# Kernel optimization log

Hardware: AMD Instinct MI355X
Metric: run time of the kernel (lower is better)

## Reference

```python
import jax, jax.numpy as jnp
import numpy as np

N = 100000   # num nodes (in_channels)
D = 128      # out_channels
H = 2 * D    # hidden dim
E = 1600000  # num edges


def gcn_conv(x, W, b, src, dst, dinv):
    """PyG GCNConv: linear -> symmetric-normalized aggregation (with self loops) -> +bias."""
    xw = x @ W                                   # [N, out]
    norm = dinv[src] * dinv[dst]                 # [E]
    msg = xw[src] * norm[:, None]                # [E, out]  gather + scale
    agg = jax.ops.segment_sum(msg, dst, num_segments=N)  # scatter-add to targets
    agg = agg + xw * (dinv * dinv)[:, None]      # self-loop contribution
    return agg + b


def setup_inputs() -> dict:
    key = jax.random.key(0)
    k1, k2, k3, k4, k5, k6 = jax.random.split(key, 6)
    emb = jax.random.normal(k1, (N, D), dtype=jnp.float32)
    # Glorot-ish scaled weights
    W1 = jax.random.normal(k2, (D, H), dtype=jnp.float32) * (1.0 / np.sqrt(D))
    b1 = jnp.zeros((H,), dtype=jnp.float32)
    W2 = jax.random.normal(k3, (H, D), dtype=jnp.float32) * (1.0 / np.sqrt(H))
    b2 = jnp.zeros((D,), dtype=jnp.float32)
    edge_index = jax.random.randint(k4, (2, E), 0, N, dtype=jnp.int32).astype(jnp.int64)
    return {"emb": emb, "W1": W1, "b1": b1, "W2": W2, "b2": b2, "edge_index": edge_index}


def reference(emb, W1, b1, W2, b2, edge_index):
    src = edge_index[0]
    dst = edge_index[1]
    # degrees include the self loop added by GCNConv (add_self_loops=True)
    deg = jax.ops.segment_sum(jnp.ones((E,), dtype=emb.dtype), dst, num_segments=N) + 1.0
    dinv = jax.lax.rsqrt(deg)                    # deg >= 1, always finite
    x = gcn_conv(emb, W1, b1, src, dst, dinv)    # [N, 2D]
    x = jax.nn.relu(x)
    out = gcn_conv(x, W2, b2, src, dst, dinv)    # [N, D]
    return out
```

## Files before the change

### kernel.cpp

```cpp
#include <hip/hip_runtime.h>
#include <hip/hip_bf16.h>

#define NN 100000
#define DD 128
#define HH 256

#define NBKT 391
#define ABLK 256

typedef _Float16 half_t;
typedef _Float16 half8 __attribute__((ext_vector_type(8)));
typedef _Float16 half4_t __attribute__((ext_vector_type(4)));
typedef float floatx4 __attribute__((ext_vector_type(4)));


__global__ __launch_bounds__(256) void hist_bkt(const int* __restrict__ dst,
                                                int* __restrict__ cnt,
                                                int* __restrict__ tot,
                                                int E, int epb) {
    __shared__ int h[NBKT];
    for (int i = threadIdx.x; i < NBKT; i += 256) h[i] = 0;
    __syncthreads();
    int base = blockIdx.x * epb;
    int end = min(base + epb, E);
    for (int e = base + (int)threadIdx.x; e < end; e += 256)
        atomicAdd(&h[dst[e] >> 8], 1);
    __syncthreads();
    for (int i = threadIdx.x; i < NBKT; i += 256) {
        int v = h[i];
        cnt[i * ABLK + blockIdx.x] = v;
        if (v) atomicAdd(&tot[i], v);
    }
}

__global__ __launch_bounds__(512) void scan_all(const int* __restrict__ tot,
                                                const int* __restrict__ cnt,
                                                int* __restrict__ bktStart,
                                                int* __restrict__ blockOff) {
    __shared__ int s[512];
    int b = blockIdx.x, t = threadIdx.x;
    int v = (t < NBKT) ? tot[t] : 0;
    s[t] = v;
    __syncthreads();
    for (int off = 1; off < 512; off <<= 1) {
        int u = (t >= off) ? s[t - off] : 0;
        __syncthreads();
        s[t] += u;
        __syncthreads();
    }
    int bs = (b > 0) ? s[b - 1] : 0;
    int tail = s[NBKT - 1];
    __syncthreads();
    if (t == 0) {
        bktStart[b] = bs;
        if (b == NBKT - 1) bktStart[NBKT] = tail;
    }
    int c = (t < ABLK) ? cnt[b * ABLK + t] : 0;
    s[t] = c;
    __syncthreads();
    for (int off = 1; off < 512; off <<= 1) {
        int u = (t >= off) ? s[t - off] : 0;
        __syncthreads();
        s[t] += u;
        __syncthreads();
    }
    if (t < ABLK) blockOff[b * ABLK + t] = bs + s[t] - c;
}

__global__ __launch_bounds__(256) void part_edges(const int* __restrict__ src,
                                                  const int* __restrict__ dst,
                                                  const int* __restrict__ blockOff,
                                                  int* __restrict__ epk4,
                                                  int E, int epb) {
    __shared__ int lbase[NBKT];
    for (int i = threadIdx.x; i < NBKT; i += 256)
        lbase[i] = blockOff[i * ABLK + blockIdx.x];
    __syncthreads();
    int base = blockIdx.x * epb;
    int end = min(base + epb, E);
    for (int e = base + (int)threadIdx.x; e < end; e += 256) {
        int d = dst[e];
        int p = atomicAdd(&lbase[d >> 8], 1);
        epk4[p] = src[e] | ((d & 255) << 17);
    }
}

__global__ __launch_bounds__(256) void build_csr(const int* __restrict__ epk4,
                                                 const int* __restrict__ bktStart,
                                                 int* __restrict__ offsets,
                                                 float* __restrict__ dinv,
                                                 int* __restrict__ eidx, int N) {
    __shared__ int ncnt[256];
    __shared__ int noff[256];
    __shared__ int cur[256];
    int b = blockIdx.x, t = threadIdx.x;
    int n0 = b << 8;
    int estart = bktStart[b], eend = bktStart[b + 1];
    ncnt[t] = 0;
    __syncthreads();
    for (int e = estart + t; e < eend; e += 256)
        atomicAdd(&ncnt[epk4[e] >> 17], 1);
    __syncthreads();
    int c = ncnt[t];
    noff[t] = c;
    __syncthreads();
    for (int off = 1; off < 256; off <<= 1) {
        int u = (t >= off) ? noff[t - off] : 0;
        __syncthreads();
        noff[t] += u;
        __syncthreads();
    }
    int myoff = estart + noff[t] - c;
    cur[t] = myoff;
    int node = n0 + t;
    if (node < N) {
        offsets[node] = myoff;
        dinv[node] = rsqrtf((float)c + 1.0f);
        if (node == N - 1) offsets[N] = eend;
    }
    __syncthreads();
    for (int e = estart + t; e < eend; e += 256) {
        int p = epk4[e];
        int pos = atomicAdd(&cur[p >> 17], 1);
        eidx[pos] = p & 0x1FFFF;
    }
}

__global__ __launch_bounds__(256) void f2h_scale(const float* __restrict__ in,
                                                 const float* __restrict__ dinv,
                                                 half_t* __restrict__ out, int n4) {
    int i = blockIdx.x * 256 + threadIdx.x;
    if (i < n4) {
        float s = dinv[i >> 5];
        float4 v = ((const float4*)in)[i];
        half4_t o = {(half_t)(v.x * s), (half_t)(v.y * s), (half_t)(v.z * s), (half_t)(v.w * s)};
        ((half4_t*)out)[i] = o;
    }
}

__global__ __launch_bounds__(256) void transpose_both(const float* __restrict__ W1,
                                                      const float* __restrict__ W2,
                                                      half_t* __restrict__ W1t,
                                                      half_t* __restrict__ W2t) {
    int i = blockIdx.x * 256 + threadIdx.x;
    if (i < DD * HH) {
        int k = i / HH, c = i - k * HH;
        W1t[(size_t)c * DD + k] = (half_t)W1[i];
    } else if (i < 2 * DD * HH) {
        int j = i - DD * HH;
        int k = j / DD, c = j - k * DD;
        W2t[(size_t)c * HH + k] = (half_t)W2[j];
    }
}

template <int K, int CT, int NCB, bool BIASRELU>
__global__ __launch_bounds__(256) void gemm_mfma(const half_t* __restrict__ A,
                                                 const half_t* __restrict__ Bt,
                                                 const float* __restrict__ dinv,
                                                 const float* __restrict__ bias,
                                                 half_t* __restrict__ C, int M) {
    constexpr int BK = 64;
    constexpr int LDA = 72;
    __shared__ __align__(16) half_t As[128][LDA];
    __shared__ __align__(16) half_t Bs[64][LDA];

    const int tid = threadIdx.x;
    const int wave = tid >> 6, lane = tid & 63;
    const int wr = wave >> 1, wc = wave & 1;

    const int d = blockIdx.x + NCB * blockIdx.y;
    const int rp = (d / (8 * NCB)) * 8 + (d & 7);
    const int cc = (d >> 3) % NCB;
    const int row0 = rp * 128;
    const int col0 = cc * 64;
    const int lrow = lane & 15, kq = lane >> 4;

    floatx4 acc[4][2] = {};

    for (int k0 = 0; k0 < K; k0 += BK) {
#pragma unroll
        for (int i = 0; i < 4; ++i) {
            int r = (tid >> 3) + i * 32;
            int kk = (tid & 7) * 8;
            int gr = row0 + r;
            half8 v = {};
            if (gr < M) v = *(const half8*)(A + (size_t)gr * K + k0 + kk);
            *(half8*)&As[r][kk] = v;
        }
#pragma unroll
        for (int i = 0; i < 2; ++i) {
            int n = (tid >> 3) + i * 32;
            int kk = (tid & 7) * 8;
            half8 v = *(const half8*)(Bt + (size_t)(col0 + n) * K + k0 + kk);
            *(half8*)&Bs[n][kk] = v;
        }
        __syncthreads();
#pragma unroll
        for (int ks = 0; ks < 2; ++ks) {
            half8 af[4], bf[2];
#pragma unroll
            for (int i = 0; i < 4; ++i)
                af[i] = *(const half8*)&As[wr * 64 + i * 16 + lrow][ks * 32 + kq * 8];
#pragma unroll
            for (int j = 0; j < 2; ++j)
                bf[j] = *(const half8*)&Bs[wc * 32 + j * 16 + lrow][ks * 32 + kq * 8];
#pragma unroll
            for (int i = 0; i < 4; ++i)
#pragma unroll
                for (int j = 0; j < 2; ++j)
                    acc[i][j] = __builtin_amdgcn_mfma_f32_16x16x32_f16(af[i], bf[j], acc[i][j], 0, 0, 0);
        }
        __syncthreads();
    }

#pragma unroll
    for (int i = 0; i < 4; ++i) {
#pragma unroll
        for (int r = 0; r < 4; ++r) {
            int grow = row0 + wr * 64 + i * 16 + kq * 4 + r;
            if (grow < M) {
                float s = BIASRELU ? 0.f : dinv[grow];
#pragma unroll
                for (int j = 0; j < 2; ++j) {
                    int gcol = col0 + wc * 32 + j * 16 + lrow;
                    float v = acc[i][j][r];
                    if (BIASRELU) v = fmaxf(v + bias[gcol], 0.f);
                    else          v = v * s;
                    C[(size_t)grow * CT + gcol] = (half_t)v;
                }
            }
        }
    }
}

template <bool OUT16>
__global__ __launch_bounds__(256) void gather128(const half_t* __restrict__ y,
                                                 void* __restrict__ outv,
                                                 const int* __restrict__ offsets,
                                                 const int* __restrict__ eidx,
                                                 const float* __restrict__ dinv,
                                                 const float* __restrict__ bias, int N) {
    int node = blockIdx.x * 8 + (threadIdx.x >> 5);
    if (node >= N) return;
    int c = (threadIdx.x & 31) * 4;

    half4_t sv = *(const half4_t*)(y + (size_t)node * DD + c);
    float a0 = (float)sv[0], a1 = (float)sv[1], a2 = (float)sv[2], a3 = (float)sv[3];
    float b0 = 0.f, b1_ = 0.f, b2_ = 0.f, b3 = 0.f;

    int e = offsets[node];
    const int e1 = offsets[node + 1];
    for (; e + 7 < e1; e += 8) {
        int s0 = eidx[e],     s1 = eidx[e + 1], s2 = eidx[e + 2], s3 = eidx[e + 3];
        int s4 = eidx[e + 4], s5 = eidx[e + 5], s6 = eidx[e + 6], s7 = eidx[e + 7];
        half4_t v0 = *(const half4_t*)(y + (size_t)s0 * DD + c);
        half4_t v1 = *(const half4_t*)(y + (size_t)s1 * DD + c);
        half4_t v2 = *(const half4_t*)(y + (size_t)s2 * DD + c);
        half4_t v3 = *(const half4_t*)(y + (size_t)s3 * DD + c);
        half4_t v4 = *(const half4_t*)(y + (size_t)s4 * DD + c);
        half4_t v5 = *(const half4_t*)(y + (size_t)s5 * DD + c);
        half4_t v6 = *(const half4_t*)(y + (size_t)s6 * DD + c);
        half4_t v7 = *(const half4_t*)(y + (size_t)s7 * DD + c);
        a0 += (float)v0[0]; a1 += (float)v0[1]; a2 += (float)v0[2]; a3 += (float)v0[3];
        b0 += (float)v1[0]; b1_ += (float)v1[1]; b2_ += (float)v1[2]; b3 += (float)v1[3];
        a0 += (float)v2[0]; a1 += (float)v2[1]; a2 += (float)v2[2]; a3 += (float)v2[3];
        b0 += (float)v3[0]; b1_ += (float)v3[1]; b2_ += (float)v3[2]; b3 += (float)v3[3];
        a0 += (float)v4[0]; a1 += (float)v4[1]; a2 += (float)v4[2]; a3 += (float)v4[3];
        b0 += (float)v5[0]; b1_ += (float)v5[1]; b2_ += (float)v5[2]; b3 += (float)v5[3];
        a0 += (float)v6[0]; a1 += (float)v6[1]; a2 += (float)v6[2]; a3 += (float)v6[3];
        b0 += (float)v7[0]; b1_ += (float)v7[1]; b2_ += (float)v7[2]; b3 += (float)v7[3];
    }
    for (; e + 3 < e1; e += 4) {
        int s0 = eidx[e], s1 = eidx[e + 1], s2 = eidx[e + 2], s3 = eidx[e + 3];
        half4_t v0 = *(const half4_t*)(y + (size_t)s0 * DD + c);
        half4_t v1 = *(const half4_t*)(y + (size_t)s1 * DD + c);
        half4_t v2 = *(const half4_t*)(y + (size_t)s2 * DD + c);
        half4_t v3 = *(const half4_t*)(y + (size_t)s3 * DD + c);
        a0 += (float)v0[0]; a1 += (float)v0[1]; a2 += (float)v0[2]; a3 += (float)v0[3];
        b0 += (float)v1[0]; b1_ += (float)v1[1]; b2_ += (float)v1[2]; b3 += (float)v1[3];
        a0 += (float)v2[0]; a1 += (float)v2[1]; a2 += (float)v2[2]; a3 += (float)v2[3];
        b0 += (float)v3[0]; b1_ += (float)v3[1]; b2_ += (float)v3[2]; b3 += (float)v3[3];
    }
    for (; e < e1; ++e) {
        int s0 = eidx[e];
        half4_t v0 = *(const half4_t*)(y + (size_t)s0 * DD + c);
        a0 += (float)v0[0]; a1 += (float)v0[1]; a2 += (float)v0[2]; a3 += (float)v0[3];
    }

    float s = dinv[node];
    float o0 = s * (a0 + b0);
    float o1 = s * (a1 + b1_);
    float o2 = s * (a2 + b2_);
    float o3 = s * (a3 + b3);
    if (OUT16) {
        half4_t o = {(half_t)o0, (half_t)o1, (half_t)o2, (half_t)o3};
        *(half4_t*)((half_t*)outv + (size_t)node * DD + c) = o;
    } else {
        float4 bb = *(const float4*)(bias + c);
        float4 o = make_float4(o0 + bb.x, o1 + bb.y, o2 + bb.z, o3 + bb.w);
        *(float4*)((float*)outv + (size_t)node * DD + c) = o;
    }
}

extern "C" void kernel_launch(void* const* d_in, const int* in_sizes, int n_in,
                              void* d_out, int out_size, void* d_ws, size_t ws_size,
                              hipStream_t stream) {
    const float* emb = (const float*)d_in[0];
    const float* W1  = (const float*)d_in[1];
    const float* b1  = (const float*)d_in[2];
    const float* W2  = (const float*)d_in[3];
    const float* b2  = (const float*)d_in[4];
    const int*   ei  = (const int*)d_in[5];

    const int N = NN;
    const int E = in_sizes[5] / 2;
    const int* src = ei;
    const int* dst = ei + E;

    char* w = (char*)d_ws;
    float*  dinv = (float*)w;  w += 100032 * 4;
    half_t* zh   = (half_t*)w; w += (size_t)NN * DD * 2;
    half_t* g1h  = (half_t*)w; w += (size_t)NN * DD * 2;
    half_t* x1h  = (half_t*)w; w += (size_t)NN * HH * 2;
    half_t* W1t  = (half_t*)w; w += (size_t)DD * HH * 2;
    half_t* W2t  = (half_t*)w; w += (size_t)HH * DD * 2;
    int* offsets = (int*)w;    w += 100032 * 4;
    int* cnt     = (int*)w;    w += (size_t)NBKT * ABLK * 4;
    int* blockOff= (int*)w;    w += (size_t)NBKT * ABLK * 4;
    int* tot     = (int*)w;    w += 512 * 4;
    int* bktStart= (int*)w;    w += 512 * 4;
    int* epk4    = (int*)w;    w += (size_t)E * 4;
    int* eidx    = (int*)w;
    float* out   = (float*)d_out;
    half_t* y2h  = zh;

    const int epb = (E + ABLK - 1) / ABLK;

    hipMemsetAsync(tot, 0, NBKT * sizeof(int), stream);
    hist_bkt<<<ABLK, 256, 0, stream>>>(dst, cnt, tot, E, epb);
    scan_all<<<NBKT, 512, 0, stream>>>(tot, cnt, bktStart, blockOff);
    part_edges<<<ABLK, 256, 0, stream>>>(src, dst, blockOff, epk4, E, epb);
    build_csr<<<NBKT, 256, 0, stream>>>(epk4, bktStart, offsets, dinv, eidx, N);

    f2h_scale<<<(NN * DD / 4 + 255) / 256, 256, 0, stream>>>(emb, dinv, zh, NN * DD / 4);
    transpose_both<<<(2 * DD * HH + 255) / 256, 256, 0, stream>>>(W1, W2, W1t, W2t);

    const int gyp = 784;
    const int aggBlocks = (N + 7) / 8;

    gather128<true><<<aggBlocks, 256, 0, stream>>>(zh, g1h, offsets, eidx, dinv, nullptr, N);
    gemm_mfma<DD, HH, 4, true><<<dim3(4, gyp), 256, 0, stream>>>(g1h, W1t, dinv, b1, x1h, N);

    gemm_mfma<HH, DD, 2, false><<<dim3(2, gyp), 256, 0, stream>>>(x1h, W2t, dinv, nullptr, y2h, N);
    gather128<false><<<aggBlocks, 256, 0, stream>>>(y2h, (void*)out, offsets, eidx, dinv, b2, N);
}
```

Before: 359.8 us.

## Fuse weight transpose into histogram and embedding scaling into CSR build; enlarge GEMM K tile

Weight transpose/convert now runs on extra blocks appended to the histogram kernel, and the fp16 conversion of the embedding, scaled by dinv, runs at the end of build_csr using dinv held in shared memory. This removes two kernel launches and a separate read of dinv. The GEMM K tile grows from 64 to 128 and the trailing barrier is skipped on the last iteration, which means fewer barriers per tile but more shared memory per block and possibly lower occupancy.

```diff
diff --git a/kernel.cpp b/kernel.cpp
--- a/kernel.cpp
+++ b/kernel.cpp
@@ -17,8 +17,26 @@
 __global__ __launch_bounds__(256) void hist_bkt(const int* __restrict__ dst,
                                                 int* __restrict__ cnt,
                                                 int* __restrict__ tot,
+                                                const float* __restrict__ W1,
+                                                const float* __restrict__ W2,
+                                                half_t* __restrict__ W1t,
+                                                half_t* __restrict__ W2t,
                                                 int E, int epb) {
     __shared__ int h[NBKT];
+    if (blockIdx.x >= ABLK) {
+        for (int i = (blockIdx.x - ABLK) * 256 + (int)threadIdx.x;
+             i < 2 * DD * HH; i += 8 * 256) {
+            if (i < DD * HH) {
+                int k = i / HH, c = i - k * HH;
+                W1t[(size_t)c * DD + k] = (half_t)W1[i];
+            } else {
+                int j = i - DD * HH;
+                int k = j / DD, c = j - k * DD;
+                W2t[(size_t)c * HH + k] = (half_t)W2[j];
+            }
+        }
+        return;
+    }
     for (int i = threadIdx.x; i < NBKT; i += 256) h[i] = 0;
     __syncthreads();
     int base = blockIdx.x * epb;
@@ -89,10 +107,13 @@
                                                  const int* __restrict__ bktStart,
                                                  int* __restrict__ offsets,
                                                  float* __restrict__ dinv,
-                                                 int* __restrict__ eidx, int N) {
+                                                 int* __restrict__ eidx,
+                                                 const float* __restrict__ emb,
+                                                 half_t* __restrict__ zh, int N) {
     __shared__ int ncnt[256];
     __shared__ int noff[256];
     __shared__ int cur[256];
+    __shared__ float dvs[256];
     int b = blockIdx.x, t = threadIdx.x;
     int n0 = b << 8;
     int estart = bktStart[b], eend = bktStart[b + 1];
@@ -113,9 +134,11 @@
     int myoff = estart + noff[t] - c;
     cur[t] = myoff;
     int node = n0 + t;
+    float rs = rsqrtf((float)c + 1.0f);
+    dvs[t] = rs;
     if (node < N) {
         offsets[node] = myoff;
-        dinv[node] = rsqrtf((float)c + 1.0f);
+        dinv[node] = rs;
         if (node == N - 1) offsets[N] = eend;
     }
     __syncthreads();
@@ -124,32 +147,17 @@
         int pos = atomicAdd(&cur[p >> 17], 1);
         eidx[pos] = p & 0x1FFFF;
     }
-}
-
-__global__ __launch_bounds__(256) void f2h_scale(const float* __restrict__ in,
-                                                 const float* __restrict__ dinv,
-                                                 half_t* __restrict__ out, int n4) {
-    int i = blockIdx.x * 256 + threadIdx.x;
-    if (i < n4) {
-        float s = dinv[i >> 5];
-        float4 v = ((const float4*)in)[i];
-        half4_t o = {(half_t)(v.x * s), (half_t)(v.y * s), (half_t)(v.z * s), (half_t)(v.w * s)};
-        ((half4_t*)out)[i] = o;
-    }
-}
-
-__global__ __launch_bounds__(256) void transpose_both(const float* __restrict__ W1,
-                                                      const float* __restrict__ W2,
-                                                      half_t* __restrict__ W1t,
-                                                      half_t* __restrict__ W2t) {
-    int i = blockIdx.x * 256 + threadIdx.x;
-    if (i < DD * HH) {
-        int k = i / HH, c = i - k * HH;
-        W1t[(size_t)c * DD + k] = (half_t)W1[i];
-    } else if (i < 2 * DD * HH) {
-        int j = i - DD * HH;
-        int k = j / DD, c = j - k * DD;
-        W2t[(size_t)c * HH + k] = (half_t)W2[j];
+    const float4* emb4 = (const float4*)emb;
+    for (int idx = t; idx < 256 * 32; idx += 256) {
+        int row = idx >> 5;
+        int nd = n0 + row;
+        if (nd < N) {
+            float s = dvs[row];
+            float4 v = emb4[(size_t)nd * 32 + (idx & 31)];
+            half4_t o = {(half_t)(v.x * s), (half_t)(v.y * s),
+                         (half_t)(v.z * s), (half_t)(v.w * s)};
+            *(half4_t*)(zh + (size_t)nd * DD + (idx & 31) * 4) = o;
+        }
     }
 }
 
@@ -159,8 +167,8 @@
                                                  const float* __restrict__ dinv,
                                                  const float* __restrict__ bias,
                                                  half_t* __restrict__ C, int M) {
-    constexpr int BK = 64;
-    constexpr int LDA = 72;
+    constexpr int BK = 128;
+    constexpr int LDA = 136;
     __shared__ __align__(16) half_t As[128][LDA];
     __shared__ __align__(16) half_t Bs[64][LDA];
 
@@ -179,24 +187,24 @@
 
     for (int k0 = 0; k0 < K; k0 += BK) {
 #pragma unroll
-        for (int i = 0; i < 4; ++i) {
-            int r = (tid >> 3) + i * 32;
-            int kk = (tid & 7) * 8;
+        for (int i = 0; i < 8; ++i) {
+            int r = (tid >> 4) + i * 16;
+            int kk = (tid & 15) * 8;
             int gr = row0 + r;
             half8 v = {};
             if (gr < M) v = *(const half8*)(A + (size_t)gr * K + k0 + kk);
             *(half8*)&As[r][kk] = v;
         }
 #pragma unroll
-        for (int i = 0; i < 2; ++i) {
-            int n = (tid >> 3) + i * 32;
-            int kk = (tid & 7) * 8;
+        for (int i = 0; i < 4; ++i) {
+            int n = (tid >> 4) + i * 16;
+            int kk = (tid & 15) * 8;
             half8 v = *(const half8*)(Bt + (size_t)(col0 + n) * K + k0 + kk);
             *(half8*)&Bs[n][kk] = v;
         }
         __syncthreads();
 #pragma unroll
-        for (int ks = 0; ks < 2; ++ks) {
+        for (int ks = 0; ks < 4; ++ks) {
             half8 af[4], bf[2];
 #pragma unroll
             for (int i = 0; i < 4; ++i)
@@ -210,7 +218,7 @@
                 for (int j = 0; j < 2; ++j)
                     acc[i][j] = __builtin_amdgcn_mfma_f32_16x16x32_f16(af[i], bf[j], acc[i][j], 0, 0, 0);
         }
-        __syncthreads();
+        if (k0 + BK < K) __syncthreads();
     }
 
 #pragma unroll
@@ -337,13 +345,10 @@
     const int epb = (E + ABLK - 1) / ABLK;
 
     hipMemsetAsync(tot, 0, NBKT * sizeof(int), stream);
-    hist_bkt<<<ABLK, 256, 0, stream>>>(dst, cnt, tot, E, epb);
+    hist_bkt<<<ABLK + 8, 256, 0, stream>>>(dst, cnt, tot, W1, W2, W1t, W2t, E, epb);
     scan_all<<<NBKT, 512, 0, stream>>>(tot, cnt, bktStart, blockOff);
     part_edges<<<ABLK, 256, 0, stream>>>(src, dst, blockOff, epk4, E, epb);
-    build_csr<<<NBKT, 256, 0, stream>>>(epk4, bktStart, offsets, dinv, eidx, N);
-
-    f2h_scale<<<(NN * DD / 4 + 255) / 256, 256, 0, stream>>>(emb, dinv, zh, NN * DD / 4);
-    transpose_both<<<(2 * DD * HH + 255) / 256, 256, 0, stream>>>(W1, W2, W1t, W2t);
+    build_csr<<<NBKT, 256, 0, stream>>>(epk4, bktStart, offsets, dinv, eidx, emb, zh, N);
 
     const int gyp = 784;
     const int aggBlocks = (N + 7) / 8;
```

Result: slower. 384.8 us (+7.0%).

## Replace LDS-staged MFMA GEMM with register-direct 64x64-per-wave tiles

Applied to the files above, without the earlier changes.

The two dense GEMMs no longer stage A and B tiles through shared memory with barriers. Each wave now loads its A rows and B columns straight from global memory into registers and computes a 64x64 output tile, so each block covers 128x128 and the grid shrinks. This removes LDS traffic and __syncthreads, but needs many more registers (64 accumulators plus 16 B fragments), which may lower occupancy. It also drops data sharing between waves, so more reads go to cache.

```diff
diff --git a/kernel.cpp b/kernel.cpp
--- a/kernel.cpp
+++ b/kernel.cpp
@@ -154,75 +154,60 @@
 }
 
 template <int K, int CT, int NCB, bool BIASRELU>
-__global__ __launch_bounds__(256) void gemm_mfma(const half_t* __restrict__ A,
-                                                 const half_t* __restrict__ Bt,
-                                                 const float* __restrict__ dinv,
-                                                 const float* __restrict__ bias,
-                                                 half_t* __restrict__ C, int M) {
-    constexpr int BK = 64;
-    constexpr int LDA = 72;
-    __shared__ __align__(16) half_t As[128][LDA];
-    __shared__ __align__(16) half_t Bs[64][LDA];
-
+__global__ __launch_bounds__(256) void gemm_reg(const half_t* __restrict__ A,
+                                                const half_t* __restrict__ Bt,
+                                                const float* __restrict__ dinv,
+                                                const float* __restrict__ bias,
+                                                half_t* __restrict__ C, int M) {
     const int tid = threadIdx.x;
     const int wave = tid >> 6, lane = tid & 63;
-    const int wr = wave >> 1, wc = wave & 1;
+    const int wr = wave & 1, wc = wave >> 1;
 
     const int d = blockIdx.x + NCB * blockIdx.y;
     const int rp = (d / (8 * NCB)) * 8 + (d & 7);
     const int cc = (d >> 3) % NCB;
-    const int row0 = rp * 128;
-    const int col0 = cc * 64;
+    const int row0 = rp * 128 + wr * 64;
+    const int col0 = cc * 128 + wc * 64;
     const int lrow = lane & 15, kq = lane >> 4;
 
-    floatx4 acc[4][2] = {};
-
-    for (int k0 = 0; k0 < K; k0 += BK) {
+    floatx4 acc[4][4] = {};
+
+#pragma unroll
+    for (int kh = 0; kh < K; kh += 128) {
+        half8 bf[4][4];
+#pragma unroll
+        for (int j = 0; j < 4; ++j) {
+            const half_t* bp = Bt + (size_t)(col0 + j * 16 + lrow) * K + kh + kq * 8;
+#pragma unroll
+            for (int ks = 0; ks < 4; ++ks)
+                bf[j][ks] = *(const half8*)(bp + ks * 32);
+        }
 #pragma unroll
         for (int i = 0; i < 4; ++i) {
-            int r = (tid >> 3) + i * 32;
-            int kk = (tid & 7) * 8;
-            int gr = row0 + r;
-            half8 v = {};
-            if (gr < M) v = *(const half8*)(A + (size_t)gr * K + k0 + kk);
-            *(half8*)&As[r][kk] = v;
+            int gr = row0 + i * 16 + lrow;
+            const half_t* ap = A + (size_t)(gr < M ? gr : 0) * K + kh + kq * 8;
+            half8 af[4];
+#pragma unroll
+            for (int ks = 0; ks < 4; ++ks)
+                af[ks] = *(const half8*)(ap + ks * 32);
+#pragma unroll
+            for (int j = 0; j < 4; ++j)
+#pragma unroll
+                for (int ks = 0; ks < 4; ++ks)
+                    acc[i][j] = __builtin_amdgcn_mfma_f32_16x16x32_f16(af[ks], bf[j][ks], acc[i][j], 0, 0, 0);
         }
-#pragma unroll
-        for (int i = 0; i < 2; ++i) {
-            int n = (tid >> 3) + i * 32;
-            int kk = (tid & 7) * 8;
-            half8 v = *(const half8*)(Bt + (size_t)(col0 + n) * K + k0 + kk);
-            *(half8*)&Bs[n][kk] = v;
-        }
-        __syncthreads();
-#pragma unroll
-        for (int ks = 0; ks < 2; ++ks) {
-            half8 af[4], bf[2];
-#pragma unroll
-            for (int i = 0; i < 4; ++i)
-                af[i] = *(const half8*)&As[wr * 64 + i * 16 + lrow][ks * 32 + kq * 8];
-#pragma unroll
-            for (int j = 0; j < 2; ++j)
-                bf[j] = *(const half8*)&Bs[wc * 32 + j * 16 + lrow][ks * 32 + kq * 8];
-#pragma unroll
-            for (int i = 0; i < 4; ++i)
-#pragma unroll
-                for (int j = 0; j < 2; ++j)
-                    acc[i][j] = __builtin_amdgcn_mfma_f32_16x16x32_f16(af[i], bf[j], acc[i][j], 0, 0, 0);
-        }
-        __syncthreads();
     }
 
 #pragma unroll
     for (int i = 0; i < 4; ++i) {
 #pragma unroll
         for (int r = 0; r < 4; ++r) {
-            int grow = row0 + wr * 64 + i * 16 + kq * 4 + r;
+            int grow = row0 + i * 16 + kq * 4 + r;
             if (grow < M) {
                 float s = BIASRELU ? 0.f : dinv[grow];
 #pragma unroll
-                for (int j = 0; j < 2; ++j) {
-                    int gcol = col0 + wc * 32 + j * 16 + lrow;
+                for (int j = 0; j < 4; ++j) {
+                    int gcol = col0 + j * 16 + lrow;
                     float v = acc[i][j][r];
                     if (BIASRELU) v = fmaxf(v + bias[gcol], 0.f);
                     else          v = v * s;
@@ -349,8 +334,8 @@
     const int aggBlocks = (N + 7) / 8;
 
     gather128<true><<<aggBlocks, 256, 0, stream>>>(zh, g1h, offsets, eidx, dinv, nullptr, N);
-    gemm_mfma<DD, HH, 4, true><<<dim3(4, gyp), 256, 0, stream>>>(g1h, W1t, dinv, b1, x1h, N);
-
-    gemm_mfma<HH, DD, 2, false><<<dim3(2, gyp), 256, 0, stream>>>(x1h, W2t, dinv, nullptr, y2h, N);
+    gemm_reg<DD, HH, 2, true><<<dim3(2, gyp), 256, 0, stream>>>(g1h, W1t, dinv, b1, x1h, N);
+
+    gemm_reg<HH, DD, 1, false><<<dim3(1, gyp), 256, 0, stream>>>(x1h, W2t, dinv, nullptr, y2h, N);
     gather128<false><<<aggBlocks, 256, 0, stream>>>(y2h, (void*)out, offsets, eidx, dinv, b2, N);
 }
```

Result: slower. 382.5 us (+6.3%).
